# Kernel tuning notes

Hardware: AMD Instinct MI355X
Metric: run time of the kernel (lower is better)

Reference implementation:

```python
import jax, jax.numpy as jnp
import numpy as np

N_NETS = 76  # 29 h2o + 13 o3 + 9 co2 + 3 n2o + 9 ch4 + 13 u
N_CH = 29
N_KE = [29, 13, 9, 3, 9, 13]
# which composition column each of the 76 nets is scaled by
GAS_OF_NET = np.repeat(np.arange(6), N_KE)
# which output channel each of the 76 tau terms is added into (hardcoded table in subcall)
CHAN_OF_NET = np.concatenate([
    np.arange(29),                                            # h2o[i] -> channel i
    np.array([0, 1, 2, 17, 18, 19, 20, 21, 22, 25, 26, 27, 28]),  # o3
    np.array([0, 1, 2, 5, 6, 9, 10, 13, 14]),                 # co2
    np.array([0, 1, 2]),                                      # n2o
    np.array([0, 1, 2, 3, 4, 7, 8, 11, 12]),                  # ch4
    np.array([0, 1, 2, 15, 16, 17, 18, 19, 20, 21, 22, 27, 28]),  # u
])


def setup_inputs() -> dict:
    key = jax.random.key(0)
    ks = jax.random.split(key, 16)
    B, D_IN, H = 262144, 2, 4
    t_p = jax.random.normal(ks[0], (B, D_IN), dtype=jnp.float32)
    composition = jax.random.uniform(ks[1], (B, 8), dtype=jnp.float32)
    null_lw = jnp.zeros((B, 1), dtype=jnp.float32)
    null_iw = jnp.zeros((B, 1), dtype=jnp.float32)
    # stacked params of the 76 tiny DenseFFNs (hidden [4,4], elu; out 1, softplus)
    W1 = jax.random.normal(ks[2], (N_NETS, D_IN, H), dtype=jnp.float32) * 0.5
    b1 = jax.random.normal(ks[3], (N_NETS, H), dtype=jnp.float32) * 0.05
    W2 = jax.random.normal(ks[4], (N_NETS, H, H), dtype=jnp.float32) * 0.5
    b2 = jax.random.normal(ks[5], (N_NETS, H), dtype=jnp.float32) * 0.05
    W3 = jax.random.uniform(ks[6], (N_NETS, H, 1), minval=-1.0, maxval=1.0, dtype=jnp.float32)
    b3 = jnp.zeros((N_NETS, 1), dtype=jnp.float32)
    # per-channel lw / iw Dense(1) layers (input dim 1)
    W_lw = jax.random.normal(ks[7], (N_CH,), dtype=jnp.float32) * 0.5
    b_lw = jax.random.uniform(ks[8], (N_CH,), minval=0.0, maxval=1.0, dtype=jnp.float32)
    W_iw = jax.random.normal(ks[9], (N_CH,), dtype=jnp.float32) * 0.5
    b_iw = jax.random.uniform(ks[10], (N_CH,), minval=0.0, maxval=1.0, dtype=jnp.float32)
    return {"t_p": t_p, "composition": composition, "null_lw": null_lw, "null_iw": null_iw,
            "W1": W1, "b1": b1, "W2": W2, "b2": b2, "W3": W3, "b3": b3,
            "W_lw": W_lw, "b_lw": b_lw, "W_iw": W_iw, "b_iw": b_iw}


def reference(t_p, composition, null_lw, null_iw, W1, b1, W2, b2, W3, b3, W_lw, b_lw, W_iw, b_iw):
    # all 76 tiny MLPs batched as one einsum chain: [n_nets, B, h]
    h = jax.nn.elu(jnp.einsum('bi,nio->nbo', t_p, W1) + b1[:, None, :])
    h = jax.nn.elu(jnp.einsum('nbi,nio->nbo', h, W2) + b2[:, None, :])
    ke = jax.nn.softplus(jnp.einsum('nbi,nio->nbo', h, W3) + b3[:, None, :])[..., 0]  # [76, B]
    # scale each net's output by its gas concentration, then scatter-add into 29 channels
    tau = ke * composition[:, GAS_OF_NET].T                                  # [76, B]
    tau_gases = jax.ops.segment_sum(tau, jnp.asarray(CHAN_OF_NET), num_segments=N_CH)  # [29, B]
    tau_gases = jnp.transpose(tau_gases)[:, :, None]                          # [B, 29, 1]
    # lw / iw: softplus(null * w_c + b_c) * composition[:, 6 or 7]
    tau_lw = (jax.nn.softplus(null_lw * W_lw[None, :] + b_lw[None, :]) * composition[:, 6:7])[:, :, None]
    tau_iw = (jax.nn.softplus(null_iw * W_iw[None, :] + b_iw[None, :]) * composition[:, 7:8])[:, :, None]
    return (tau_gases, tau_lw, tau_iw)
```

## Files before the change

kernel.cpp:

```cpp
#include <hip/hip_runtime.h>
#include <hip/hip_fp16.h>
#include <cstdint>

#define BLOCK 256
#define ROWS 64
#define NRECU 40

typedef float v4f __attribute__((ext_vector_type(4)));
typedef _Float16 h2 __attribute__((ext_vector_type(2)));

__device__ __forceinline__ float exp2s(float x) { return __builtin_amdgcn_exp2f(x); }
__device__ __forceinline__ float log2s(float x) { return __builtin_amdgcn_logf(x); }

__device__ __forceinline__ h2 fmah(h2 a, h2 b, h2 c) { return __builtin_elementwise_fma(a, b, c); }
__device__ __forceinline__ h2 maxh(h2 a, h2 b) { return __builtin_elementwise_max(a, b); }
__device__ __forceinline__ h2 minh(h2 a, h2 b) { return __builtin_elementwise_min(a, b); }

union h2u { h2 h; uint32_t u; __half2 hh; };

__device__ __forceinline__ h2 exp2h(h2 x) {
    h2u a; a.h = x;
    h2u r; r.hh = h2exp2(a.hh);
    return r.h;
}
__device__ __forceinline__ h2 splath(float s) {
    const _Float16 v = (_Float16)s;
    return (h2){v, v};
}

#define LN2 0.6931471805599453f
#define L2E 1.4426950408889634f

constexpr int GAS_[76] = {
    0,0,0,0,0,0,0,0,0,0,0,0,0,0,0,0,0,0,0,0,0,0,0,0,0,0,0,0,0,
    1,1,1,1,1,1,1,1,1,1,1,1,1,
    2,2,2,2,2,2,2,2,2,
    3,3,3,
    4,4,4,4,4,4,4,4,4,
    5,5,5,5,5,5,5,5,5,5,5,5,5};
constexpr int CHAN_[76] = {
    0,1,2,3,4,5,6,7,8,9,10,11,12,13,14,15,16,17,18,19,20,21,22,23,24,25,26,27,28,
    0,1,2,17,18,19,20,21,22,25,26,27,28,
    0,1,2,5,6,9,10,13,14,
    0,1,2,
    0,1,2,3,4,7,8,11,12,
    0,1,2,15,16,17,18,19,20,21,22,27,28};

__global__ void __launch_bounds__(128)
prep_kernel(const float* __restrict__ W1, const float* __restrict__ b1,
            const float* __restrict__ W2, const float* __restrict__ b2,
            const float* __restrict__ W3, const float* __restrict__ b3,
            const float* __restrict__ W_lw, const float* __restrict__ b_lw,
            const float* __restrict__ W_iw, const float* __restrict__ b_iw,
            float* __restrict__ rec)
{
    const int p = threadIdx.x;
    if (p < 38) {
        const int nA = 2 * p, nB = 2 * p + 1;
        uint32_t* r = (uint32_t*)rec + p * NRECU;
        auto pack = [](float a, float b) -> uint32_t {
            h2u v; v.h = (h2){(_Float16)a, (_Float16)b};
            return v.u;
        };
        #pragma unroll
        for (int k = 0; k < 8; ++k)
            r[k] = pack(W1[nA * 8 + k] * L2E, W1[nB * 8 + k] * L2E);
        #pragma unroll
        for (int o = 0; o < 4; ++o)
            r[8 + o] = pack(b1[nA * 4 + o] * L2E, b1[nB * 4 + o] * L2E);
        #pragma unroll
        for (int k = 0; k < 16; ++k)
            r[12 + k] = pack(W2[nA * 16 + k] * L2E, W2[nB * 16 + k] * L2E);
        #pragma unroll
        for (int o = 0; o < 4; ++o) {
            float sA = 0.0f, sB = 0.0f;
            #pragma unroll
            for (int i = 0; i < 4; ++i) {
                sA += W2[nA * 16 + i * 4 + o];
                sB += W2[nB * 16 + i * 4 + o];
            }
            r[28 + o] = pack((b2[nA * 4 + o] - sA) * L2E, (b2[nB * 4 + o] - sB) * L2E);
        }
        float s3A = 0.0f, s3B = 0.0f;
        #pragma unroll
        for (int i = 0; i < 4; ++i) {
            r[32 + i] = pack(W3[nA * 4 + i] * L2E, W3[nB * 4 + i] * L2E);
            s3A += W3[nA * 4 + i];
            s3B += W3[nB * 4 + i];
        }
        r[36] = pack((b3[nA] - s3A) * L2E, (b3[nB] - s3B) * L2E);
        r[37] = 0u; r[38] = 0u; r[39] = 0u;
    } else if (p < 38 + 29) {
        const int ch = p - 38;
        float* t = rec + 38 * NRECU + ch * 4;
        t[0] = W_lw[ch] * L2E;
        t[1] = b_lw[ch] * L2E;
        t[2] = W_iw[ch] * L2E;
        t[3] = b_iw[ch] * L2E;
    }
}

__device__ __forceinline__ h2 elu_h16(h2 as) {
    return maxh(fmah(as, splath(LN2), splath(1.0f)), exp2h(minh(as, splath(0.0f))));
}

template<int PS, int PE>
__device__ __forceinline__ void run_pairs(
    const uint32_t* __restrict__ recU, h2 tpx2, h2 tpy2,
    const float* cgl2 , float* tau)
{
    #pragma unroll
    for (int p = PS; p < PE; ++p) {
        const h2* __restrict__ RP = (const h2*)(recU + p * NRECU);
        h2 H1[4];
        #pragma unroll
        for (int o = 0; o < 4; ++o)
            H1[o] = elu_h16(fmah(tpx2, RP[o], fmah(tpy2, RP[4 + o], RP[8 + o])));
        h2 H2[4];
        #pragma unroll
        for (int o = 0; o < 4; ++o) {
            h2 a = RP[28 + o];
            #pragma unroll
            for (int i = 0; i < 4; ++i)
                a = fmah(H1[i], RP[12 + i * 4 + o], a);
            H2[o] = elu_h16(a);
        }
        h2 a3 = RP[36];
        #pragma unroll
        for (int i = 0; i < 4; ++i)
            a3 = fmah(H2[i], RP[32 + i], a3);
        const float ax = (float)a3.x;
        const float ay = (float)a3.y;
        const float spx = fmaxf(ax, 0.0f) + log2s(1.0f + exp2s(-fabsf(ax)));
        const float spy = fmaxf(ay, 0.0f) + log2s(1.0f + exp2s(-fabsf(ay)));
        tau[CHAN_[2 * p]]     = fmaf(spx, cgl2[GAS_[2 * p]],     tau[CHAN_[2 * p]]);
        tau[CHAN_[2 * p + 1]] = fmaf(spy, cgl2[GAS_[2 * p + 1]], tau[CHAN_[2 * p + 1]]);
    }
}

template<bool EXACT>
__global__ void __launch_bounds__(BLOCK)
od_kernel(const float* __restrict__ t_p,
          const float* __restrict__ comp,
          const float* __restrict__ null_lw,
          const float* __restrict__ null_iw,
          const float* __restrict__ rec,
          float* __restrict__ out, int B)
{
    __shared__ float stage[2][ROWS * 29];

    const int tid  = threadIdx.x;
    const int wave = tid >> 6;
    const int lane = tid & 63;
    const int base = blockIdx.x * ROWS;
    const int row  = EXACT ? (base + lane)
                           : ((base + lane < B) ? (base + lane) : (B - 1));

    const float2 tp = *reinterpret_cast<const float2*>(t_p + (size_t)row * 2);
    const float4 ca = *reinterpret_cast<const float4*>(comp + (size_t)row * 8);
    const float2 cb = *reinterpret_cast<const float2*>(comp + (size_t)row * 8 + 4);
    const float cgl2[6] = {ca.x * LN2, ca.y * LN2, ca.z * LN2,
                           ca.w * LN2, cb.x * LN2, cb.y * LN2};

    const h2 tpx2 = splath(tp.x);
    const h2 tpy2 = splath(tp.y);

    float tau[29];
    #pragma unroll
    for (int i = 0; i < 29; ++i) tau[i] = 0.0f;

    const uint32_t* __restrict__ recU = (const uint32_t*)rec;

    switch (wave) {
        case 0: run_pairs< 0, 10>(recU, tpx2, tpy2, cgl2, tau); break;
        case 1: run_pairs<10, 20>(recU, tpx2, tpy2, cgl2, tau); break;
        case 2: run_pairs<20, 29>(recU, tpx2, tpy2, cgl2, tau); break;
        default: run_pairs<29, 38>(recU, tpx2, tpy2, cgl2, tau); break;
    }

    if (wave < 2) {
        #pragma unroll
        for (int i = 0; i < 29; ++i) stage[wave][lane * 29 + i] = tau[i];
    }
    __syncthreads();
    if (wave >= 2) {
        float* p = stage[wave - 2];
        #pragma unroll
        for (int i = 0; i < 29; ++i) p[lane * 29 + i] += tau[i];
    }
    __syncthreads();

    const size_t obase = (size_t)base * 29;
    const size_t BN = (size_t)B * 29;
    const float* __restrict__ recL = rec + 38 * NRECU;

    if (EXACT) {
        const int t4 = tid * 4;
        #pragma unroll
        for (int it = 0; it < 2; ++it) {
            const int idx = t4 + it * (BLOCK * 4);
            if (idx < ROWS * 29) {
                const v4f s0 = *reinterpret_cast<const v4f*>(&stage[0][idx]);
                const v4f s1 = *reinterpret_cast<const v4f*>(&stage[1][idx]);
                const v4f v0 = s0 + s1;

                float o1[4], o2[4];
                int rr = idx / 29;
                int cc = idx - rr * 29;
                #pragma unroll
                for (int j = 0; j < 4; ++j) {
                    const int grow = base + rr;
                    const float nl = null_lw[grow];
                    const float ni = null_iw[grow];
                    const float c6 = comp[(size_t)grow * 8 + 6] * LN2;
                    const float c7 = comp[(size_t)grow * 8 + 7] * LN2;
                    const v4f L = *reinterpret_cast<const v4f*>(recL + cc * 4);
                    const float alw = fmaf(nl, L.x, L.y);
                    const float aiw = fmaf(ni, L.z, L.w);
                    o1[j] = (fmaxf(alw, 0.0f) + log2s(1.0f + exp2s(-fabsf(alw)))) * c6;
                    o2[j] = (fmaxf(aiw, 0.0f) + log2s(1.0f + exp2s(-fabsf(aiw)))) * c7;
                    if (++cc == 29) { cc = 0; ++rr; }
                }
                const v4f v1 = {o1[0], o1[1], o1[2], o1[3]};
                const v4f v2 = {o2[0], o2[1], o2[2], o2[3]};
                __builtin_nontemporal_store(v0, reinterpret_cast<v4f*>(out + obase + idx));
                __builtin_nontemporal_store(v1, reinterpret_cast<v4f*>(out + BN + obase + idx));
                __builtin_nontemporal_store(v2, reinterpret_cast<v4f*>(out + 2 * BN + obase + idx));
            }
        }
    } else {
        const int rrem0 = B - base;
        const int rrem = rrem0 < 0 ? 0 : (rrem0 > ROWS ? ROWS : rrem0);
        const int lim = rrem * 29;
        for (int idx = tid; idx < lim; idx += BLOCK) {
            out[obase + idx] = stage[0][idx] + stage[1][idx];
            const int r  = idx / 29;
            const int ch = idx - r * 29;
            const int grow = base + r;
            const float nl = null_lw[grow];
            const float ni = null_iw[grow];
            const float c6 = comp[(size_t)grow * 8 + 6] * LN2;
            const float c7 = comp[(size_t)grow * 8 + 7] * LN2;
            const v4f L = *reinterpret_cast<const v4f*>(recL + ch * 4);
            const float alw = fmaf(nl, L.x, L.y);
            const float aiw = fmaf(ni, L.z, L.w);
            out[BN + obase + idx] =
                (fmaxf(alw, 0.0f) + log2s(1.0f + exp2s(-fabsf(alw)))) * c6;
            out[2 * BN + obase + idx] =
                (fmaxf(aiw, 0.0f) + log2s(1.0f + exp2s(-fabsf(aiw)))) * c7;
        }
    }
}

extern "C" void kernel_launch(void* const* d_in, const int* in_sizes, int n_in,
                              void* d_out, int out_size, void* d_ws, size_t ws_size,
                              hipStream_t stream) {
    const float* t_p     = (const float*)d_in[0];
    const float* comp    = (const float*)d_in[1];
    const float* null_lw = (const float*)d_in[2];
    const float* null_iw = (const float*)d_in[3];
    const float* W1      = (const float*)d_in[4];
    const float* b1      = (const float*)d_in[5];
    const float* W2      = (const float*)d_in[6];
    const float* b2      = (const float*)d_in[7];
    const float* W3      = (const float*)d_in[8];
    const float* b3      = (const float*)d_in[9];
    const float* W_lw    = (const float*)d_in[10];
    const float* b_lw    = (const float*)d_in[11];
    const float* W_iw    = (const float*)d_in[12];
    const float* b_iw    = (const float*)d_in[13];
    float* out = (float*)d_out;
    float* rec = (float*)d_ws;

    const int B = in_sizes[0] / 2;

    prep_kernel<<<1, 128, 0, stream>>>(W1, b1, W2, b2, W3, b3,
                                       W_lw, b_lw, W_iw, b_iw, rec);

    const int blocks = (B + ROWS - 1) / ROWS;
    if (B % ROWS == 0)
        od_kernel<true><<<blocks, BLOCK, 0, stream>>>(t_p, comp, null_lw, null_iw,
                                                      rec, out, B);
    else
        od_kernel<false><<<blocks, BLOCK, 0, stream>>>(t_p, comp, null_lw, null_iw,
                                                       rec, out, B);
}
```

Before: 51.99 us.

## Process two rows per thread to amortize weight loads and use packed FP32 FMA

```diff
diff --git a/kernel.cpp b/kernel.cpp
--- a/kernel.cpp
+++ b/kernel.cpp
@@ -3,14 +3,16 @@
 #include <cstdint>
 
 #define BLOCK 256
-#define ROWS 64
+#define ROWS 128
 #define NRECU 40
 
+typedef float v2f __attribute__((ext_vector_type(2)));
 typedef float v4f __attribute__((ext_vector_type(4)));
 typedef _Float16 h2 __attribute__((ext_vector_type(2)));
 
 __device__ __forceinline__ float exp2s(float x) { return __builtin_amdgcn_exp2f(x); }
 __device__ __forceinline__ float log2s(float x) { return __builtin_amdgcn_logf(x); }
+__device__ __forceinline__ v2f fma2(v2f a, v2f b, v2f c) { return __builtin_elementwise_fma(a, b, c); }
 
 __device__ __forceinline__ h2 fmah(h2 a, h2 b, h2 c) { return __builtin_elementwise_fma(a, b, c); }
 __device__ __forceinline__ h2 maxh(h2 a, h2 b) { return __builtin_elementwise_max(a, b); }
@@ -105,36 +107,48 @@
 }
 
 template<int PS, int PE>
-__device__ __forceinline__ void run_pairs(
-    const uint32_t* __restrict__ recU, h2 tpx2, h2 tpy2,
-    const float* cgl2 , float* tau)
+__device__ __forceinline__ void run_pairs2(
+    const uint32_t* __restrict__ recU,
+    h2 tpxa, h2 tpya, h2 tpxb, h2 tpyb,
+    const v2f* cgl2 , v2f* tau)
 {
     #pragma unroll
     for (int p = PS; p < PE; ++p) {
         const h2* __restrict__ RP = (const h2*)(recU + p * NRECU);
-        h2 H1[4];
-        #pragma unroll
-        for (int o = 0; o < 4; ++o)
-            H1[o] = elu_h16(fmah(tpx2, RP[o], fmah(tpy2, RP[4 + o], RP[8 + o])));
-        h2 H2[4];
+        h2 H1a[4], H1b[4];
         #pragma unroll
         for (int o = 0; o < 4; ++o) {
-            h2 a = RP[28 + o];
-            #pragma unroll
-            for (int i = 0; i < 4; ++i)
-                a = fmah(H1[i], RP[12 + i * 4 + o], a);
-            H2[o] = elu_h16(a);
-        }
-        h2 a3 = RP[36];
-        #pragma unroll
-        for (int i = 0; i < 4; ++i)
-            a3 = fmah(H2[i], RP[32 + i], a3);
-        const float ax = (float)a3.x;
-        const float ay = (float)a3.y;
-        const float spx = fmaxf(ax, 0.0f) + log2s(1.0f + exp2s(-fabsf(ax)));
-        const float spy = fmaxf(ay, 0.0f) + log2s(1.0f + exp2s(-fabsf(ay)));
-        tau[CHAN_[2 * p]]     = fmaf(spx, cgl2[GAS_[2 * p]],     tau[CHAN_[2 * p]]);
-        tau[CHAN_[2 * p + 1]] = fmaf(spy, cgl2[GAS_[2 * p + 1]], tau[CHAN_[2 * p + 1]]);
+            H1a[o] = elu_h16(fmah(tpxa, RP[o], fmah(tpya, RP[4 + o], RP[8 + o])));
+            H1b[o] = elu_h16(fmah(tpxb, RP[o], fmah(tpyb, RP[4 + o], RP[8 + o])));
+        }
+        h2 H2a[4], H2b[4];
+        #pragma unroll
+        for (int o = 0; o < 4; ++o) {
+            h2 aa = RP[28 + o];
+            h2 ab = RP[28 + o];
+            #pragma unroll
+            for (int i = 0; i < 4; ++i) {
+                aa = fmah(H1a[i], RP[12 + i * 4 + o], aa);
+                ab = fmah(H1b[i], RP[12 + i * 4 + o], ab);
+            }
+            H2a[o] = elu_h16(aa);
+            H2b[o] = elu_h16(ab);
+        }
+        h2 a3a = RP[36];
+        h2 a3b = RP[36];
+        #pragma unroll
+        for (int i = 0; i < 4; ++i) {
+            a3a = fmah(H2a[i], RP[32 + i], a3a);
+            a3b = fmah(H2b[i], RP[32 + i], a3b);
+        }
+        const float ax0 = (float)a3a.x, ay0 = (float)a3a.y;
+        const float ax1 = (float)a3b.x, ay1 = (float)a3b.y;
+        const v2f sp0 = {fmaxf(ax0, 0.0f) + log2s(1.0f + exp2s(-fabsf(ax0))),
+                         fmaxf(ax1, 0.0f) + log2s(1.0f + exp2s(-fabsf(ax1)))};
+        const v2f sp1 = {fmaxf(ay0, 0.0f) + log2s(1.0f + exp2s(-fabsf(ay0))),
+                         fmaxf(ay1, 0.0f) + log2s(1.0f + exp2s(-fabsf(ay1)))};
+        tau[CHAN_[2 * p]]     = fma2(sp0, cgl2[GAS_[2 * p]],     tau[CHAN_[2 * p]]);
+        tau[CHAN_[2 * p + 1]] = fma2(sp1, cgl2[GAS_[2 * p + 1]], tau[CHAN_[2 * p + 1]]);
     }
 }
 
@@ -147,108 +161,122 @@
           const float* __restrict__ rec,
           float* __restrict__ out, int B)
 {
-    __shared__ float stage[2][ROWS * 29];
+    __shared__ float stage[2][64 * 29];
 
     const int tid  = threadIdx.x;
     const int wave = tid >> 6;
     const int lane = tid & 63;
     const int base = blockIdx.x * ROWS;
-    const int row  = EXACT ? (base + lane)
-                           : ((base + lane < B) ? (base + lane) : (B - 1));
-
-    const float2 tp = *reinterpret_cast<const float2*>(t_p + (size_t)row * 2);
-    const float4 ca = *reinterpret_cast<const float4*>(comp + (size_t)row * 8);
-    const float2 cb = *reinterpret_cast<const float2*>(comp + (size_t)row * 8 + 4);
-    const float cgl2[6] = {ca.x * LN2, ca.y * LN2, ca.z * LN2,
-                           ca.w * LN2, cb.x * LN2, cb.y * LN2};
-
-    const h2 tpx2 = splath(tp.x);
-    const h2 tpy2 = splath(tp.y);
-
-    float tau[29];
+    int r0 = base + lane;
+    int r1 = base + 64 + lane;
+    if (!EXACT) { r0 = r0 < B ? r0 : B - 1; r1 = r1 < B ? r1 : B - 1; }
+
+    const float2 ta = *reinterpret_cast<const float2*>(t_p + (size_t)r0 * 2);
+    const float2 tb = *reinterpret_cast<const float2*>(t_p + (size_t)r1 * 2);
+    const float4 ca0 = *reinterpret_cast<const float4*>(comp + (size_t)r0 * 8);
+    const float2 cb0 = *reinterpret_cast<const float2*>(comp + (size_t)r0 * 8 + 4);
+    const float4 ca1 = *reinterpret_cast<const float4*>(comp + (size_t)r1 * 8);
+    const float2 cb1 = *reinterpret_cast<const float2*>(comp + (size_t)r1 * 8 + 4);
+    const v2f cgl2[6] = {
+        {ca0.x * LN2, ca1.x * LN2}, {ca0.y * LN2, ca1.y * LN2},
+        {ca0.z * LN2, ca1.z * LN2}, {ca0.w * LN2, ca1.w * LN2},
+        {cb0.x * LN2, cb1.x * LN2}, {cb0.y * LN2, cb1.y * LN2}};
+
+    const h2 tpxa = splath(ta.x), tpya = splath(ta.y);
+    const h2 tpxb = splath(tb.x), tpyb = splath(tb.y);
+
+    v2f tau[29];
     #pragma unroll
-    for (int i = 0; i < 29; ++i) tau[i] = 0.0f;
+    for (int i = 0; i < 29; ++i) tau[i] = (v2f){0.0f, 0.0f};
 
     const uint32_t* __restrict__ recU = (const uint32_t*)rec;
 
     switch (wave) {
-        case 0: run_pairs< 0, 10>(recU, tpx2, tpy2, cgl2, tau); break;
-        case 1: run_pairs<10, 20>(recU, tpx2, tpy2, cgl2, tau); break;
-        case 2: run_pairs<20, 29>(recU, tpx2, tpy2, cgl2, tau); break;
-        default: run_pairs<29, 38>(recU, tpx2, tpy2, cgl2, tau); break;
+        case 0: run_pairs2< 0, 10>(recU, tpxa, tpya, tpxb, tpyb, cgl2, tau); break;
+        case 1: run_pairs2<10, 20>(recU, tpxa, tpya, tpxb, tpyb, cgl2, tau); break;
+        case 2: run_pairs2<20, 29>(recU, tpxa, tpya, tpxb, tpyb, cgl2, tau); break;
+        default: run_pairs2<29, 38>(recU, tpxa, tpya, tpxb, tpyb, cgl2, tau); break;
     }
 
-    if (wave < 2) {
-        #pragma unroll
-        for (int i = 0; i < 29; ++i) stage[wave][lane * 29 + i] = tau[i];
-    }
-    __syncthreads();
-    if (wave >= 2) {
-        float* p = stage[wave - 2];
-        #pragma unroll
-        for (int i = 0; i < 29; ++i) p[lane * 29 + i] += tau[i];
-    }
-    __syncthreads();
-
-    const size_t obase = (size_t)base * 29;
     const size_t BN = (size_t)B * 29;
     const float* __restrict__ recL = rec + 38 * NRECU;
 
-    if (EXACT) {
-        const int t4 = tid * 4;
-        #pragma unroll
-        for (int it = 0; it < 2; ++it) {
-            const int idx = t4 + it * (BLOCK * 4);
-            if (idx < ROWS * 29) {
-                const v4f s0 = *reinterpret_cast<const v4f*>(&stage[0][idx]);
-                const v4f s1 = *reinterpret_cast<const v4f*>(&stage[1][idx]);
-                const v4f v0 = s0 + s1;
-
-                float o1[4], o2[4];
-                int rr = idx / 29;
-                int cc = idx - rr * 29;
-                #pragma unroll
-                for (int j = 0; j < 4; ++j) {
-                    const int grow = base + rr;
-                    const float nl = null_lw[grow];
-                    const float ni = null_iw[grow];
-                    const float c6 = comp[(size_t)grow * 8 + 6] * LN2;
-                    const float c7 = comp[(size_t)grow * 8 + 7] * LN2;
-                    const v4f L = *reinterpret_cast<const v4f*>(recL + cc * 4);
-                    const float alw = fmaf(nl, L.x, L.y);
-                    const float aiw = fmaf(ni, L.z, L.w);
-                    o1[j] = (fmaxf(alw, 0.0f) + log2s(1.0f + exp2s(-fabsf(alw)))) * c6;
-                    o2[j] = (fmaxf(aiw, 0.0f) + log2s(1.0f + exp2s(-fabsf(aiw)))) * c7;
-                    if (++cc == 29) { cc = 0; ++rr; }
+    #pragma unroll
+    for (int pass = 0; pass < 2; ++pass) {
+        if (wave < 2) {
+            #pragma unroll
+            for (int i = 0; i < 29; ++i)
+                stage[wave][lane * 29 + i] = pass ? tau[i].y : tau[i].x;
+        }
+        __syncthreads();
+        if (wave >= 2) {
+            float* p = stage[wave - 2];
+            #pragma unroll
+            for (int i = 0; i < 29; ++i)
+                p[lane * 29 + i] += pass ? tau[i].y : tau[i].x;
+        }
+        __syncthreads();
+
+        const int pbase = base + pass * 64;
+        const size_t obase = (size_t)pbase * 29;
+
+        if (EXACT) {
+            const int t4 = tid * 4;
+            #pragma unroll
+            for (int it = 0; it < 2; ++it) {
+                const int idx = t4 + it * (BLOCK * 4);
+                if (idx < 64 * 29) {
+                    const v4f s0 = *reinterpret_cast<const v4f*>(&stage[0][idx]);
+                    const v4f s1 = *reinterpret_cast<const v4f*>(&stage[1][idx]);
+                    const v4f v0 = s0 + s1;
+
+                    float o1[4], o2[4];
+                    int rr = idx / 29;
+                    int cc = idx - rr * 29;
+                    #pragma unroll
+                    for (int j = 0; j < 4; ++j) {
+                        const int grow = pbase + rr;
+                        const float nl = null_lw[grow];
+                        const float ni = null_iw[grow];
+                        const float c6 = comp[(size_t)grow * 8 + 6] * LN2;
+                        const float c7 = comp[(size_t)grow * 8 + 7] * LN2;
+                        const v4f L = *reinterpret_cast<const v4f*>(recL + cc * 4);
+                        const float alw = fmaf(nl, L.x, L.y);
+                        const float aiw = fmaf(ni, L.z, L.w);
+                        o1[j] = (fmaxf(alw, 0.0f) + log2s(1.0f + exp2s(-fabsf(alw)))) * c6;
+                        o2[j] = (fmaxf(aiw, 0.0f) + log2s(1.0f + exp2s(-fabsf(aiw)))) * c7;
+                        if (++cc == 29) { cc = 0; ++rr; }
+                    }
+                    const v4f v1 = {o1[0], o1[1], o1[2], o1[3]};
+                    const v4f v2 = {o2[0], o2[1], o2[2], o2[3]};
+                    __builtin_nontemporal_store(v0, reinterpret_cast<v4f*>(out + obase + idx));
+                    __builtin_nontemporal_store(v1, reinterpret_cast<v4f*>(out + BN + obase + idx));
+                    __builtin_nontemporal_store(v2, reinterpret_cast<v4f*>(out + 2 * BN + obase + idx));
                 }
-                const v4f v1 = {o1[0], o1[1], o1[2], o1[3]};
-                const v4f v2 = {o2[0], o2[1], o2[2], o2[3]};
-                __builtin_nontemporal_store(v0, reinterpret_cast<v4f*>(out + obase + idx));
-                __builtin_nontemporal_store(v1, reinterpret_cast<v4f*>(out + BN + obase + idx));
-                __builtin_nontemporal_store(v2, reinterpret_cast<v4f*>(out + 2 * BN + obase + idx));
             }
-        }
-    } else {
-        const int rrem0 = B - base;
-        const int rrem = rrem0 < 0 ? 0 : (rrem0 > ROWS ? ROWS : rrem0);
-        const int lim = rrem * 29;
-        for (int idx = tid; idx < lim; idx += BLOCK) {
-            out[obase + idx] = stage[0][idx] + stage[1][idx];
-            const int r  = idx / 29;
-            const int ch = idx - r * 29;
-            const int grow = base + r;
-            const float nl = null_lw[grow];
-            const float ni = null_iw[grow];
-            const float c6 = comp[(size_t)grow * 8 + 6] * LN2;
-            const float c7 = comp[(size_t)grow * 8 + 7] * LN2;
-            const v4f L = *reinterpret_cast<const v4f*>(recL + ch * 4);
-            const float alw = fmaf(nl, L.x, L.y);
-            const float aiw = fmaf(ni, L.z, L.w);
-            out[BN + obase + idx] =
-                (fmaxf(alw, 0.0f) + log2s(1.0f + exp2s(-fabsf(alw)))) * c6;
-            out[2 * BN + obase + idx] =
-                (fmaxf(aiw, 0.0f) + log2s(1.0f + exp2s(-fabsf(aiw)))) * c7;
-        }
+        } else {
+            int rrem = B - pbase;
+            rrem = rrem < 0 ? 0 : (rrem > 64 ? 64 : rrem);
+            const int lim = rrem * 29;
+            for (int idx = tid; idx < lim; idx += BLOCK) {
+                out[obase + idx] = stage[0][idx] + stage[1][idx];
+                const int r  = idx / 29;
+                const int ch = idx - r * 29;
+                const int grow = pbase + r;
+                const float nl = null_lw[grow];
+                const float ni = null_iw[grow];
+                const float c6 = comp[(size_t)grow * 8 + 6] * LN2;
+                const float c7 = comp[(size_t)grow * 8 + 7] * LN2;
+                const v4f L = *reinterpret_cast<const v4f*>(recL + ch * 4);
+                const float alw = fmaf(nl, L.x, L.y);
+                const float aiw = fmaf(ni, L.z, L.w);
+                out[BN + obase + idx] =
+                    (fmaxf(alw, 0.0f) + log2s(1.0f + exp2s(-fabsf(alw)))) * c6;
+                out[2 * BN + obase + idx] =
+                    (fmaxf(aiw, 0.0f) + log2s(1.0f + exp2s(-fabsf(aiw)))) * c7;
+            }
+        }
+        if (pass == 0) __syncthreads();
     }
 }
 
```

Measured after the change: 52.49 us. Within noise of the previous version (+1.0%).
